# Performance work log

Measured on AMD Instinct MI355X. Metric: run time of the kernel, lower is better.

The kernel has to match this reference:

```python
import jax, jax.numpy as jnp
import numpy as np


def setup_inputs() -> dict:
    key = jax.random.key(0)
    kx, kg = jax.random.split(key)
    x = jax.random.normal(kx, (16, 512, 64, 64), dtype=jnp.float32)
    gamma = jax.random.normal(kg, (1,), dtype=jnp.float32)
    return {"x": x, "gamma": gamma}


def reference(x, gamma):
    B, C, H, W = x.shape
    q = x.reshape(B, C, H * W)                      # [B, C, N]
    # energy[b, c, d] = <channel c, channel d> over spatial positions
    energy = jnp.einsum('bcn,bdn->bcd', q, q)       # [B, C, C]
    # max-centering softmax: softmax(rowmax(energy) - energy)
    energy_new = jnp.max(energy, axis=-1, keepdims=True) - energy
    attention = jax.nn.softmax(energy_new, axis=-1)  # [B, C, C]
    out = jnp.einsum('bcd,bdn->bcn', attention, q).reshape(B, C, H, W)
    return gamma * out + x
```

## Files before the change

kernel.cpp:

```cpp
#include <hip/hip_runtime.h>


#define BATCH 16
#define CCH   512
#define NSP   4096

typedef __attribute__((ext_vector_type(8))) short bfx8;
typedef __attribute__((ext_vector_type(4))) float fx4;
typedef __attribute__((ext_vector_type(2))) float fx2;
typedef __attribute__((ext_vector_type(4))) int   ix4;

__device__ __forceinline__ short f2bf(float v) {
    union { float f; unsigned u; } a; a.f = v;
    unsigned r = a.u + 0x7fffu + ((a.u >> 16) & 1u);
    return (short)(r >> 16);
}

__device__ __forceinline__ void gload16(const short* g, short* l) {
    __builtin_amdgcn_global_load_lds((const __attribute__((address_space(1))) void*)g,
                                     (__attribute__((address_space(3))) void*)l, 16, 0, 0);
}
__device__ __forceinline__ void gload16c(const char* g, char* l) {
    __builtin_amdgcn_global_load_lds((const __attribute__((address_space(1))) void*)g,
                                     (__attribute__((address_space(3))) void*)l, 16, 0, 0);
}

__global__ __launch_bounds__(256) void fused_split_kernel(const float* __restrict__ x,
                                                          char* __restrict__ xa,
                                                          char* __restrict__ xb,
                                                          short* __restrict__ xt) {
    int blk = blockIdx.x;
    int b  = blk >> 9;
    int t  = blk & 511;
    int ct = t >> 6;
    int nt = t & 63;
    int c0 = ct * 64, n0 = nt * 64;
    const float* xbp = x  + (size_t)b * CCH * NSP;
    char*        xab = xa + (size_t)b * CCH * NSP;
    char*        xbb = xb + (size_t)b * CCH * NSP;
    short*       xtb = xt + (size_t)b * NSP * CCH;

    __shared__ short A[64][64];
    __shared__ short Bn[64][64];

    int tid = threadIdx.x;

#pragma unroll
    for (int s = 0; s < 2; ++s) {
        int idx = s * 256 + tid;
        int row = idx >> 3;
        int ch  = idx & 7;
        const float* p = xbp + (size_t)(c0 + row) * NSP + n0 + ch * 8;
        fx4 v0 = *(const fx4*)p;
        fx4 v1 = *(const fx4*)(p + 4);
        int av[8], bv[8];
        bfx8 h;
#pragma unroll
        for (int e = 0; e < 4; ++e) {
            float xv = v0[e];
            h[e] = f2bf(xv);
            float xs = fminf(fmaxf(xv * 2048.0f, -16384.0f), 16319.0f);
            int q = __float2int_rn(xs);
            int aq = (q + 64) >> 7;
            av[e] = aq; bv[e] = q - (aq << 7);
            xv = v1[e];
            h[e + 4] = f2bf(xv);
            xs = fminf(fmaxf(xv * 2048.0f, -16384.0f), 16319.0f);
            q = __float2int_rn(xs);
            aq = (q + 64) >> 7;
            av[e + 4] = aq; bv[e + 4] = q - (aq << 7);
        }
        unsigned pa0 = (unsigned)(av[0] & 255) | ((unsigned)(av[1] & 255) << 8) |
                       ((unsigned)(av[2] & 255) << 16) | ((unsigned)(av[3] & 255) << 24);
        unsigned pa1 = (unsigned)(av[4] & 255) | ((unsigned)(av[5] & 255) << 8) |
                       ((unsigned)(av[6] & 255) << 16) | ((unsigned)(av[7] & 255) << 24);
        unsigned pb0 = (unsigned)(bv[0] & 255) | ((unsigned)(bv[1] & 255) << 8) |
                       ((unsigned)(bv[2] & 255) << 16) | ((unsigned)(bv[3] & 255) << 24);
        unsigned pb1 = (unsigned)(bv[4] & 255) | ((unsigned)(bv[5] & 255) << 8) |
                       ((unsigned)(bv[6] & 255) << 16) | ((unsigned)(bv[7] & 255) << 24);
        size_t go = (size_t)(c0 + row) * NSP + n0 + ch * 8;
        ((unsigned*)(xab + go))[0] = pa0; ((unsigned*)(xab + go))[1] = pa1;
        ((unsigned*)(xbb + go))[0] = pb0; ((unsigned*)(xbb + go))[1] = pb1;
        *(bfx8*)(&A[row][(ch ^ (row & 7)) * 8]) = h;
    }
    __syncthreads();

    int p  = tid & 31;
    int dr = tid >> 5;
    unsigned wv[8];
#pragma unroll
    for (int i = 0; i < 8; ++i) {
        int r = dr * 8 + i;
        int byte = r * 128 + ((((p >> 2) ^ (r & 7)) * 8 + (2 * p & 7)) * 2);
        wv[i] = *(const unsigned*)((const char*)&A[0][0] + byte);
    }
    bfx8 q0, q1;
#pragma unroll
    for (int i = 0; i < 8; ++i) { q0[i] = (short)(wv[i] & 0xffff); q1[i] = (short)(wv[i] >> 16); }

    int slot2 = dr ^ (p & 7);
    *(bfx8*)(&Bn[2 * p][slot2 * 8])     = q0;
    *(bfx8*)(&Bn[2 * p + 1][slot2 * 8]) = q1;
    __syncthreads();

#pragma unroll
    for (int it = 0; it < 2; ++it) {
        int n  = it * 32 + (tid >> 3);
        int ch = tid & 7;
        bfx8 v = *(const bfx8*)(&Bn[n][(ch ^ ((n >> 1) & 7)) * 8]);
        __builtin_nontemporal_store(v, (bfx8*)(xtb + (size_t)(n0 + n) * CCH + c0 + ch * 8));
    }
}

__global__ __launch_bounds__(256) void energy_kernel(const char* __restrict__ xa,
                                                     const char* __restrict__ xb,
                                                     float* __restrict__ energy) {
    int orig = blockIdx.x;
    int wgid = (orig & 7) * 72 + (orig >> 3);
    int b = wgid / 36;
    int t = wgid % 36;
    int ti = 0, rem = t;
    while (rem >= 8 - ti) { rem -= 8 - ti; ++ti; }
    int tj = ti + rem;
    int c0 = ti * 64, d0 = tj * 64;
    bool diag = (ti == tj);
    const char* pa = xa + (size_t)b * CCH * NSP;
    const char* pb = xb + (size_t)b * CCH * NSP;

    __shared__ char S[2][4][32][128];

    int tid  = threadIdx.x;
    int lane = tid & 63;
    int w    = tid >> 6;
    int wr   = (w >> 1) * 32;
    int wc   = (w & 1) * 32;

    int pp  = lane >> 3;
    int e0i = (lane & 7) ^ pp;
    int ehi = e0i >> 2, kg = e0i & 3;
    const char* ssrc = (w & 1) ? pb : pa;
    int rbase = (w >= 2) ? d0 : c0;
    bool doStage = (w < 2) || !diag;

    auto STAGE = [&](int buf, int kt) {
        if (!doStage) return;
#pragma unroll
        for (int s = 0; s < 4; ++s) {
            int r = 16 * s + 2 * pp + ehi;
            gload16c(ssrc + (size_t)(rbase + r) * NSP + kt * 64 + kg * 16, &S[buf][w][s * 8][0]);
        }
    };

    ix4 acc1[2][2], acc2[2][2], acc3[2][2];
#pragma unroll
    for (int i = 0; i < 2; i++)
#pragma unroll
        for (int j = 0; j < 2; j++) { acc1[i][j] = (ix4)(0); acc2[i][j] = (ix4)(0); acc3[i][j] = (ix4)(0); }

    STAGE(0, 0);
    __syncthreads();

    int m = lane & 15, kgrp = lane >> 4;
    int slot16 = (((kgrp + 4 * (m & 1)) ^ (m >> 1)) << 4);
    int phalf  = m >> 1;
    int aBa = diag ? 0 : 2, aBb = diag ? 1 : 3;

    int cur = 0;
    const int NT = NSP / 64;
    for (int kt = 0; kt < NT; ++kt) {
        ix4 faa[2], fab[2], fba[2], fbb[2];
#pragma unroll
        for (int mi = 0; mi < 2; ++mi) {
            int p = (wr >> 1) + mi * 8 + phalf;
            faa[mi] = *(const ix4*)&S[cur][0][p][slot16];
            fab[mi] = *(const ix4*)&S[cur][1][p][slot16];
        }
#pragma unroll
        for (int ni = 0; ni < 2; ++ni) {
            int p = (wc >> 1) + ni * 8 + phalf;
            fba[ni] = *(const ix4*)&S[cur][aBa][p][slot16];
            fbb[ni] = *(const ix4*)&S[cur][aBb][p][slot16];
        }
        if (kt + 1 < NT) STAGE(cur ^ 1, kt + 1);
        __builtin_amdgcn_s_setprio(1);
#pragma unroll
        for (int mi = 0; mi < 2; ++mi)
#pragma unroll
            for (int ni = 0; ni < 2; ++ni) {
                acc1[mi][ni] = __builtin_amdgcn_mfma_i32_16x16x64_i8(faa[mi], fba[ni], acc1[mi][ni], 0, 0, 0);
                acc2[mi][ni] = __builtin_amdgcn_mfma_i32_16x16x64_i8(faa[mi], fbb[ni], acc2[mi][ni], 0, 0, 0);
                acc2[mi][ni] = __builtin_amdgcn_mfma_i32_16x16x64_i8(fab[mi], fba[ni], acc2[mi][ni], 0, 0, 0);
                acc3[mi][ni] = __builtin_amdgcn_mfma_i32_16x16x64_i8(fab[mi], fbb[ni], acc3[mi][ni], 0, 0, 0);
            }
        __builtin_amdgcn_s_setprio(0);
        __syncthreads();
        cur ^= 1;
    }

    int colw = lane & 15;
    int rowg = (lane >> 4) * 4;
#pragma unroll
    for (int mi = 0; mi < 2; ++mi)
#pragma unroll
        for (int ni = 0; ni < 2; ++ni) {
            int cb = c0 + wr + mi * 16 + rowg;
            int d  = d0 + wc + ni * 16 + colw;
#pragma unroll
            for (int r = 0; r < 4; ++r) {
                int c = cb + r;
                float v = (float)acc1[mi][ni][r] * 0.00390625f
                        + (float)acc2[mi][ni][r] * 3.0517578125e-05f
                        + (float)acc3[mi][ni][r] * 2.384185791015625e-07f;
                energy[((size_t)b * CCH + c) * CCH + d] = v;
                if (!diag)
                    energy[((size_t)b * CCH + d) * CCH + c] = v;
            }
        }
}

__global__ __launch_bounds__(256) void softmax_kernel(float* __restrict__ energy) {
    size_t row = blockIdx.x;
    float* e = energy + row * CCH;
    int tid = threadIdx.x;
    fx2 v = *(const fx2*)(e + 2 * tid);

    float m = fminf(v[0], v[1]);
#pragma unroll
    for (int off = 32; off; off >>= 1) m = fminf(m, __shfl_xor(m, off));
    __shared__ float redm[4];
    __shared__ float reds[4];
    if ((tid & 63) == 0) redm[tid >> 6] = m;
    __syncthreads();
    m = fminf(fminf(redm[0], redm[1]), fminf(redm[2], redm[3]));

    float w0 = __expf(m - v[0]);
    float w1 = __expf(m - v[1]);
    float s = w0 + w1;
#pragma unroll
    for (int off = 32; off; off >>= 1) s += __shfl_xor(s, off);
    if ((tid & 63) == 0) reds[tid >> 6] = s;
    __syncthreads();
    s = (reds[0] + reds[1]) + (reds[2] + reds[3]);
    float inv = 1.0f / s;
    unsigned uw = ((unsigned)(unsigned short)f2bf(w0 * inv)) |
                  (((unsigned)(unsigned short)f2bf(w1 * inv)) << 16);
    ((unsigned*)e)[tid] = uw;
}

__global__ __launch_bounds__(256, 4) void out_kernel(const float* __restrict__ x,
                                                     const short* __restrict__ attnb,
                                                     const short* __restrict__ xt,
                                                     const float* __restrict__ gamma,
                                                     float* __restrict__ out) {
    int orig = blockIdx.x;
    int blk  = (orig & 7) * 256 + (orig >> 3);
    int b   = blk >> 7;
    int t   = blk & 127;
    int c0  = (t >> 5) * 128;
    int n0  = (t & 31) * 128;
    const float* xb = x + (size_t)b * CCH * NSP;
    const short* ab = attnb + (size_t)b * CCH * 1024;
    const short* qt = xt + (size_t)b * NSP * CCH;

    __shared__ short SA[2][128][32];
    __shared__ short SB[2][128][32];

    int tid  = threadIdx.x;
    int lane = tid & 63;
    int w    = tid >> 6;
    int wr   = (w >> 1) * 64;
    int wc   = (w & 1) * 64;

    int srow = lane >> 2;
    int gch  = (lane & 3) ^ ((lane >> 3) & 3);

    auto STAGE = [&](int buf, int kt) {
#pragma unroll
        for (int hf = 0; hf < 2; ++hf) {
            int rg = hf * 64 + w * 16;
            gload16(ab + (size_t)(c0 + rg + srow) * 1024 + kt * 32 + gch * 8, &SA[buf][rg][0]);
            gload16(qt + (size_t)(n0 + rg + srow) * 512  + kt * 32 + gch * 8, &SB[buf][rg][0]);
        }
    };

    fx4 acc[4][4];
#pragma unroll
    for (int i = 0; i < 4; i++)
#pragma unroll
        for (int j = 0; j < 4; j++) acc[i][j] = (fx4)(0.0f);

    STAGE(0, 0);
    __syncthreads();

    int h = lane >> 4;
    int cur = 0;
    const int NT = CCH / 32;
    for (int kt = 0; kt < NT; ++kt) {
        if (kt + 1 < NT) STAGE(cur ^ 1, kt + 1);

        bfx8 af[4], bf[4];
#pragma unroll
        for (int mi = 0; mi < 4; ++mi) {
            int r  = wr + mi * 16 + (lane & 15);
            af[mi] = *(const bfx8*)((const char*)&SA[cur][0][0] + r * 64 + ((h ^ ((r >> 1) & 3)) << 4));
        }
#pragma unroll
        for (int ni = 0; ni < 4; ++ni) {
            int r  = wc + ni * 16 + (lane & 15);
            bf[ni] = *(const bfx8*)((const char*)&SB[cur][0][0] + r * 64 + ((h ^ ((r >> 1) & 3)) << 4));
        }
        __builtin_amdgcn_s_setprio(1);
#pragma unroll
        for (int mi = 0; mi < 4; ++mi)
#pragma unroll
            for (int ni = 0; ni < 4; ++ni)
                acc[mi][ni] = __builtin_amdgcn_mfma_f32_16x16x32_bf16(af[mi], bf[ni], acc[mi][ni], 0, 0, 0);
        __builtin_amdgcn_s_setprio(0);
        __syncthreads();
        cur ^= 1;
    }

    float g = gamma[0];
    int colw = lane & 15;
    int rowg = (lane >> 4) * 4;
#pragma unroll
    for (int mi = 0; mi < 4; ++mi)
#pragma unroll
        for (int ni = 0; ni < 4; ++ni) {
            int n = n0 + wc + ni * 16 + colw;
#pragma unroll
            for (int r = 0; r < 4; ++r) {
                int c = c0 + wr + mi * 16 + rowg + r;
                size_t off = ((size_t)b * CCH + c) * NSP + n;
                out[off] = g * acc[mi][ni][r] + xb[(size_t)c * NSP + n];
            }
        }
}

extern "C" void kernel_launch(void* const* d_in, const int* in_sizes, int n_in,
                              void* d_out, int out_size, void* d_ws, size_t ws_size,
                              hipStream_t stream) {
    (void)in_sizes; (void)n_in; (void)out_size; (void)ws_size;
    const float* x     = (const float*)d_in[0];
    const float* gamma = (const float*)d_in[1];
    float*       out   = (float*)d_out;

    size_t nel = (size_t)BATCH * CCH * NSP;
    char*  xap = (char*)d_ws;
    char*  xbp = xap + nel;
    short* xtp = (short*)(xap + 2 * nel);
    float* e0  = (float*)(xap + 4 * nel);

    fused_split_kernel<<<BATCH * 512, 256, 0, stream>>>(x, xap, xbp, xtp);
    energy_kernel     <<<BATCH * 36, 256, 0, stream>>>(xap, xbp, e0);
    softmax_kernel    <<<BATCH * CCH, 256, 0, stream>>>(e0);
    out_kernel        <<<BATCH * 128, 256, 0, stream>>>(x, (const short*)e0, xtp, gamma, out);
}
```

Before: 204.1 us.

## Load out_kernel MFMA operands directly from global into registers, dropping LDS staging

The out_kernel GEMM no longer stages A (attention) and B (transposed x) tiles through double-buffered shared memory with barriers. Each lane now loads its MFMA fragments straight from global memory into registers, using a two-deep register ping-pong for prefetch. The launch-bounds occupancy hint is lowered from 4 to 3 to leave room for the extra registers. This removes LDS traffic and __syncthreads, but data shared between waves is now fetched separately by each wave, which leans on L1/L2 for reuse, and the global accesses are less coalesced.

```diff
diff --git a/kernel.cpp b/kernel.cpp
--- a/kernel.cpp
+++ b/kernel.cpp
@@ -16,10 +16,6 @@
     return (short)(r >> 16);
 }
 
-__device__ __forceinline__ void gload16(const short* g, short* l) {
-    __builtin_amdgcn_global_load_lds((const __attribute__((address_space(1))) void*)g,
-                                     (__attribute__((address_space(3))) void*)l, 16, 0, 0);
-}
 __device__ __forceinline__ void gload16c(const char* g, char* l) {
     __builtin_amdgcn_global_load_lds((const __attribute__((address_space(1))) void*)g,
                                      (__attribute__((address_space(3))) void*)l, 16, 0, 0);
@@ -247,7 +243,7 @@
     ((unsigned*)e)[tid] = uw;
 }
 
-__global__ __launch_bounds__(256, 4) void out_kernel(const float* __restrict__ x,
+__global__ __launch_bounds__(256, 3) void out_kernel(const float* __restrict__ x,
                                                      const short* __restrict__ attnb,
                                                      const short* __restrict__ xt,
                                                      const float* __restrict__ gamma,
@@ -262,26 +258,23 @@
     const short* ab = attnb + (size_t)b * CCH * 1024;
     const short* qt = xt + (size_t)b * NSP * CCH;
 
-    __shared__ short SA[2][128][32];
-    __shared__ short SB[2][128][32];
-
     int tid  = threadIdx.x;
     int lane = tid & 63;
     int w    = tid >> 6;
     int wr   = (w >> 1) * 64;
     int wc   = (w & 1) * 64;
 
-    int srow = lane >> 2;
-    int gch  = (lane & 3) ^ ((lane >> 3) & 3);
-
-    auto STAGE = [&](int buf, int kt) {
-#pragma unroll
-        for (int hf = 0; hf < 2; ++hf) {
-            int rg = hf * 64 + w * 16;
-            gload16(ab + (size_t)(c0 + rg + srow) * 1024 + kt * 32 + gch * 8, &SA[buf][rg][0]);
-            gload16(qt + (size_t)(n0 + rg + srow) * 512  + kt * 32 + gch * 8, &SB[buf][rg][0]);
-        }
-    };
+    int fm = lane & 15;
+    int kg = lane >> 4;
+
+    const short* pA[4];
+    const short* pB[4];
+#pragma unroll
+    for (int mi = 0; mi < 4; ++mi)
+        pA[mi] = ab + (size_t)(c0 + wr + mi * 16 + fm) * 1024 + kg * 8;
+#pragma unroll
+    for (int ni = 0; ni < 4; ++ni)
+        pB[ni] = qt + (size_t)(n0 + wc + ni * 16 + fm) * 512 + kg * 8;
 
     fx4 acc[4][4];
 #pragma unroll
@@ -289,35 +282,37 @@
 #pragma unroll
         for (int j = 0; j < 4; j++) acc[i][j] = (fx4)(0.0f);
 
-    STAGE(0, 0);
-    __syncthreads();
-
-    int h = lane >> 4;
-    int cur = 0;
+    bfx8 a0[4], b0[4], a1[4], b1[4];
+#pragma unroll
+    for (int i = 0; i < 4; ++i) { a0[i] = *(const bfx8*)(pA[i]); b0[i] = *(const bfx8*)(pB[i]); }
+
     const int NT = CCH / 32;
-    for (int kt = 0; kt < NT; ++kt) {
-        if (kt + 1 < NT) STAGE(cur ^ 1, kt + 1);
-
-        bfx8 af[4], bf[4];
-#pragma unroll
-        for (int mi = 0; mi < 4; ++mi) {
-            int r  = wr + mi * 16 + (lane & 15);
-            af[mi] = *(const bfx8*)((const char*)&SA[cur][0][0] + r * 64 + ((h ^ ((r >> 1) & 3)) << 4));
-        }
-#pragma unroll
-        for (int ni = 0; ni < 4; ++ni) {
-            int r  = wc + ni * 16 + (lane & 15);
-            bf[ni] = *(const bfx8*)((const char*)&SB[cur][0][0] + r * 64 + ((h ^ ((r >> 1) & 3)) << 4));
-        }
-        __builtin_amdgcn_s_setprio(1);
+#pragma unroll 1
+    for (int kt = 0; kt < NT; kt += 2) {
+        if (kt + 1 < NT) {
+#pragma unroll
+            for (int i = 0; i < 4; ++i) {
+                a1[i] = *(const bfx8*)(pA[i] + (kt + 1) * 32);
+                b1[i] = *(const bfx8*)(pB[i] + (kt + 1) * 32);
+            }
+        }
 #pragma unroll
         for (int mi = 0; mi < 4; ++mi)
 #pragma unroll
             for (int ni = 0; ni < 4; ++ni)
-                acc[mi][ni] = __builtin_amdgcn_mfma_f32_16x16x32_bf16(af[mi], bf[ni], acc[mi][ni], 0, 0, 0);
-        __builtin_amdgcn_s_setprio(0);
-        __syncthreads();
-        cur ^= 1;
+                acc[mi][ni] = __builtin_amdgcn_mfma_f32_16x16x32_bf16(a0[mi], b0[ni], acc[mi][ni], 0, 0, 0);
+        if (kt + 2 < NT) {
+#pragma unroll
+            for (int i = 0; i < 4; ++i) {
+                a0[i] = *(const bfx8*)(pA[i] + (kt + 2) * 32);
+                b0[i] = *(const bfx8*)(pB[i] + (kt + 2) * 32);
+            }
+        }
+#pragma unroll
+        for (int mi = 0; mi < 4; ++mi)
+#pragma unroll
+            for (int ni = 0; ni < 4; ++ni)
+                acc[mi][ni] = __builtin_amdgcn_mfma_f32_16x16x32_bf16(a1[mi], b1[ni], acc[mi][ni], 0, 0, 0);
     }
 
     float g = gamma[0];
```

Measured after the change: 277.4 us. 1.36x slower.
